# Kernel tuning notes

Measured on AMD Instinct MI355X. Metric: run time of the kernel, lower is better.

The kernel has to match this reference:

```python
import jax, jax.numpy as jnp
from jax import lax
import numpy as np

P_NUM = 63
CHANNEL = 64
KSIZE = 5
PAD = KSIZE // 2
MEAN = jnp.linspace(-310.0, 310.0, P_NUM).reshape(1, 1, P_NUM, 1, 1)
DN = ('NCHW', 'OIHW', 'NCHW')


def rep_pad(x, p=PAD):
    return jnp.pad(x, ((0, 0), (0, 0), (p, p), (p, p)), mode='edge')


def conv(x, w, b):
    out = lax.conv_general_dilated(x, w, (1, 1), 'VALID', dimension_numbers=DN)
    return out + b[None, :, None, None]


def conv_transpose(x, w):
    # torch conv_transpose2d with weight (in, out, k, k), stride 1, no pad ==
    # full correlation with spatially flipped, in/out-transposed kernel
    k = jnp.flip(w, (-2, -1)).transpose(1, 0, 2, 3)  # (out, in, k, k)
    kh = KSIZE - 1
    return lax.conv_general_dilated(x, k, (1, 1), [(kh, kh), (kh, kh)], dimension_numbers=DN)


def crop(x, p=PAD):
    return x[:, :, p:-p, p:-p]


def act(x, w, gradient=False):
    # x: (B,C,H,W); w: (1,C,P,1,1); Gaussian-mixture RBF activation
    d = x[:, :, None, :, :] - MEAN                 # (B,C,P,H,W)
    g = jnp.exp(d * d / -200.0)
    if gradient:
        g = g * (d / -100.0)
    return (g * w).sum(axis=2)                     # (B,C,H,W)


def setup_inputs() -> dict:
    key = jax.random.key(0)
    ks = jax.random.split(key, 8)
    B, H, W = 4, 128, 128
    return {
        'x': jax.random.uniform(ks[0], (B, 1, H, W), jnp.float32),
        'y': jax.random.uniform(ks[1], (B, 1, H, W), jnp.float32),
        'lam': 0,
        'f0': jax.random.normal(ks[2], (CHANNEL, 1, KSIZE, KSIZE), jnp.float32) * 0.1,
        'b0': jax.random.normal(ks[3], (CHANNEL,), jnp.float32) * 0.01,
        'f1': jax.random.normal(ks[4], (1, CHANNEL, KSIZE, KSIZE), jnp.float32) * 0.1,
        'b1': jax.random.normal(ks[5], (1,), jnp.float32) * 0.01,
        'w0': jax.random.normal(ks[6], (1, CHANNEL, P_NUM, 1, 1), jnp.float32) * 0.1,
        'w1': jax.random.normal(ks[7], (1, 1, P_NUM, 1, 1), jnp.float32) * 0.1,
        'lam_param': jnp.float32(np.log(0.1)),
    }


def reference(x, y, lam, f0, b0, f1, b1, w0, w1, lam_param):
    del lam  # third forward arg is ignored by the original module
    x = x * 255.0
    y = y * 255.0
    xx = x
    # encoder
    c0 = conv(rep_pad(x), f0, b0)        # (B,C,H,W)
    a0 = act(c0, w0)
    c1 = conv(rep_pad(a0), f1, b1)       # (B,1,H,W)
    a1 = act(c1, w1)
    # decoder (gradient-like path)
    d = crop(conv_transpose(a1, f1))     # (B,C,H,W)
    d = d * act(c0, w0, gradient=True)
    d = crop(conv_transpose(d, f0))      # (B,1,H,W)
    out = (xx - (d + jnp.exp(lam_param) * (xx - y))) / 255.0
    return out
```

## Files before the change

kernel.cpp:

```cpp
#include <hip/hip_runtime.h>

#define BSZ 4
#define CH 64
#define IH 128
#define IW 128
#define PN 63
#define TLS 32
#define TLH 36
#define XSD 40
#define NT 64
#define CG 8
#define NG 8
#define NPIX (BSZ*IH*IW)

__device__ __forceinline__ float wsel(const float* __restrict__ wrow, int pc, int j) {
    int p  = pc + j;
    int pi = min(max(p, 0), PN - 1);
    return (p == pi) ? wrow[pi] : 0.0f;
}

__device__ __forceinline__ void act_vg(float vv, const float* __restrict__ wrow,
                                       float& av, float& ag) {
    float pcf = floorf(__fmaf_rn(vv, 0.1f, 31.5f));
    pcf = fminf(fmaxf(pcf, 0.0f), 62.0f);
    const int pc = (int)pcf;
    float d0 = vv - __fmaf_rn(pcf, 10.0f, -310.0f);
    d0 = fminf(fmaxf(d0, -150.0f), 150.0f);
    const float G0 = __expf(d0 * d0 * -0.005f);
    const float T  = __expf(d0 * 0.1f);
    const float Ti = __expf(d0 * -0.1f);
    const float C1 = 0.60653066f, C2 = 0.13533528f, C3 = 0.011108997f, C4 = 4.0867714e-4f;
    float accv, accg;
    {
        float t = wsel(wrow, pc, 0) * G0;
        accv = t; accg = t * d0;
    }
    float Tp = T, Tm = Ti;
    {
        float gc = G0 * C1;
        float tp = wsel(wrow, pc,  1) * (gc * Tp);
        float tm = wsel(wrow, pc, -1) * (gc * Tm);
        accv += tp + tm;
        accg = __fmaf_rn(tp, d0 - 10.0f, accg);
        accg = __fmaf_rn(tm, d0 + 10.0f, accg);
    }
    Tp *= T; Tm *= Ti;
    {
        float gc = G0 * C2;
        float tp = wsel(wrow, pc,  2) * (gc * Tp);
        float tm = wsel(wrow, pc, -2) * (gc * Tm);
        accv += tp + tm;
        accg = __fmaf_rn(tp, d0 - 20.0f, accg);
        accg = __fmaf_rn(tm, d0 + 20.0f, accg);
    }
    Tp *= T; Tm *= Ti;
    {
        float gc = G0 * C3;
        float tp = wsel(wrow, pc,  3) * (gc * Tp);
        float tm = wsel(wrow, pc, -3) * (gc * Tm);
        accv += tp + tm;
        accg = __fmaf_rn(tp, d0 - 30.0f, accg);
        accg = __fmaf_rn(tm, d0 + 30.0f, accg);
    }
    Tp *= T; Tm *= Ti;
    {
        float gc = G0 * C4;
        float tp = wsel(wrow, pc,  4) * (gc * Tp);
        float tm = wsel(wrow, pc, -4) * (gc * Tm);
        accv += tp + tm;
        accg = __fmaf_rn(tp, d0 - 40.0f, accg);
        accg = __fmaf_rn(tm, d0 + 40.0f, accg);
    }
    av = accv;
    ag = accg * -0.01f;
}

__device__ __forceinline__ float act_v(float vv, const float* __restrict__ wrow) {
    float pcf = floorf(__fmaf_rn(vv, 0.1f, 31.5f));
    pcf = fminf(fmaxf(pcf, 0.0f), 62.0f);
    const int pc = (int)pcf;
    float d0 = vv - __fmaf_rn(pcf, 10.0f, -310.0f);
    d0 = fminf(fmaxf(d0, -150.0f), 150.0f);
    const float G0 = __expf(d0 * d0 * -0.005f);
    const float T  = __expf(d0 * 0.1f);
    const float Ti = __expf(d0 * -0.1f);
    const float C1 = 0.60653066f, C2 = 0.13533528f, C3 = 0.011108997f, C4 = 4.0867714e-4f;
    float accv = wsel(wrow, pc, 0) * G0;
    float Tp = T, Tm = Ti;
    accv += G0 * C1 * (wsel(wrow, pc, 1) * Tp + wsel(wrow, pc, -1) * Tm);
    Tp *= T; Tm *= Ti;
    accv += G0 * C2 * (wsel(wrow, pc, 2) * Tp + wsel(wrow, pc, -2) * Tm);
    Tp *= T; Tm *= Ti;
    accv += G0 * C3 * (wsel(wrow, pc, 3) * Tp + wsel(wrow, pc, -3) * Tm);
    Tp *= T; Tm *= Ti;
    accv += G0 * C4 * (wsel(wrow, pc, 4) * Tp + wsel(wrow, pc, -4) * Tm);
    return accv;
}

__global__ __launch_bounds__(256) void kAB(const float* __restrict__ x,
                                           const float* __restrict__ f0,
                                           const float* __restrict__ b0,
                                           const float* __restrict__ w0,
                                           const float* __restrict__ f1,
                                           float* __restrict__ c1p,
                                           float* __restrict__ g0out) {
    __shared__ float xs[XSD * XSD];
    __shared__ float a0s[CG][TLH * TLH];
    __shared__ float w0s[CG][PN];

    const int tile = blockIdx.x;
    const int cgi  = blockIdx.y;
    const int cg   = cgi * CG;
    const int b    = tile >> 4;
    const int t    = tile & 15;
    const int h0   = (t >> 2) * TLS;
    const int w0p  = (t & 3) * TLS;
    const int tid  = threadIdx.x;

    for (int i = tid; i < XSD * XSD; i += 256) {
        int iy = i / XSD, ix = i - iy * XSD;
        int gy = min(max(h0 + iy - 4, 0), IH - 1);
        int gx = min(max(w0p + ix - 4, 0), IW - 1);
        xs[i] = x[((size_t)b * IH + gy) * IW + gx] * 255.0f;
    }
    for (int i = tid; i < CG * PN; i += 256)
        w0s[i / PN][i % PN] = w0[(size_t)cg * PN + i];
    __syncthreads();

    for (int p = tid; p < TLH * TLH; p += 256) {
        const int py = p / TLH, px = p - py * TLH;
        const int gy = h0 + py - 2, gx = w0p + px - 2;
        const int gyc = min(max(gy, 0), IH - 1);
        const int gxc = min(max(gx, 0), IW - 1);
        const bool interior = (gy == gyc) && (gx == gxc);
        const int cy = gyc - h0 + 4, cx = gxc - w0p + 4;

        float win[25];
#pragma unroll
        for (int u = 0; u < 5; ++u)
#pragma unroll
            for (int v = 0; v < 5; ++v)
                win[u * 5 + v] = xs[(cy - 2 + u) * XSD + cx - 2 + v];

#pragma unroll
        for (int cc = 0; cc < CG; ++cc) {
            const int c = cg + cc;
            float acc = b0[c];
#pragma unroll
            for (int k = 0; k < 25; ++k)
                acc = __fmaf_rn(win[k], f0[(size_t)c * 25 + k], acc);
            float av, ag;
            act_vg(acc, w0s[cc], av, ag);
            a0s[cc][p] = av;
            if (interior)
                g0out[(((size_t)b * CH + c) * IH + gy) * IW + gx] = ag;
        }
    }
    __syncthreads();

    const int lx = tid & 15, ly = tid >> 4;
    const int r0 = 2 * ly, c0 = 2 * lx;
    float a00 = 0.f, a01 = 0.f, a10 = 0.f, a11 = 0.f;

#pragma unroll 2
    for (int cc = 0; cc < CG; ++cc) {
        float win[6][6];
#pragma unroll
        for (int r = 0; r < 6; ++r) {
            const float2* rp = (const float2*)&a0s[cc][(r0 + r) * TLH + c0];
            float2 p0 = rp[0], p1 = rp[1], p2 = rp[2];
            win[r][0] = p0.x; win[r][1] = p0.y; win[r][2] = p1.x;
            win[r][3] = p1.y; win[r][4] = p2.x; win[r][5] = p2.y;
        }
#pragma unroll
        for (int u = 0; u < 5; ++u)
#pragma unroll
            for (int v = 0; v < 5; ++v) {
                const float kv = f1[(size_t)(cg + cc) * 25 + u * 5 + v];
                a00 = __fmaf_rn(win[u][v],         kv, a00);
                a01 = __fmaf_rn(win[u][v + 1],     kv, a01);
                a10 = __fmaf_rn(win[u + 1][v],     kv, a10);
                a11 = __fmaf_rn(win[u + 1][v + 1], kv, a11);
            }
    }

    const int oy = h0 + r0, ox = w0p + c0;
    const size_t base = (size_t)cgi * NPIX + ((size_t)b * IH + oy) * IW + ox;
    *(float2*)&c1p[base]      = make_float2(a00, a01);
    *(float2*)&c1p[base + IW] = make_float2(a10, a11);
}

__global__ __launch_bounds__(256) void kCD(const float* __restrict__ c1p,
                                           const float* __restrict__ b1,
                                           const float* __restrict__ w1,
                                           const float* __restrict__ f1,
                                           const float* __restrict__ f0,
                                           const float* __restrict__ g0,
                                           float* __restrict__ d3p) {
    __shared__ float a1s[XSD * XSD];
    __shared__ float dbs[CG][TLH * TLH];
    __shared__ float w1s[PN];

    const int tile = blockIdx.x;
    const int cgi  = blockIdx.y;
    const int cg   = cgi * CG;
    const int b    = tile >> 4;
    const int t    = tile & 15;
    const int h0   = (t >> 2) * TLS;
    const int w0p  = (t & 3) * TLS;
    const int tid  = threadIdx.x;

    if (tid < PN) w1s[tid] = w1[tid];
    __syncthreads();

    const float b1v = b1[0];

    for (int p = tid; p < XSD * XSD; p += 256) {
        int iy = p / XSD, ix = p - iy * XSD;
        int gy = h0 + iy - 4, gx = w0p + ix - 4;
        float v = 0.0f;
        if ((unsigned)gy < IH && (unsigned)gx < IW) {
            const size_t pix = ((size_t)b * IH + gy) * IW + gx;
            float s = b1v;
#pragma unroll
            for (int g = 0; g < NG; ++g) s += c1p[(size_t)g * NPIX + pix];
            v = act_v(s, w1s);
        }
        a1s[p] = v;
    }
    __syncthreads();

    for (int p = tid; p < TLH * TLH; p += 256) {
        const int py = p / TLH, px = p - py * TLH;
        const int gy = h0 + py - 2, gx = w0p + px - 2;
        const bool inb = ((unsigned)gy < IH) && ((unsigned)gx < IW);

        float win[25];
#pragma unroll
        for (int u = 0; u < 5; ++u)
#pragma unroll
            for (int v = 0; v < 5; ++v)
                win[u * 5 + v] = a1s[(py + 4 - u) * XSD + (px + 4 - v)];

#pragma unroll
        for (int cc = 0; cc < CG; ++cc) {
            float out = 0.0f;
            if (inb) {
                const int c = cg + cc;
                float d1 = 0.0f;
#pragma unroll
                for (int k = 0; k < 25; ++k)
                    d1 = __fmaf_rn(win[k], f1[(size_t)c * 25 + k], d1);
                out = d1 * g0[(((size_t)b * CH + c) * IH + gy) * IW + gx];
            }
            dbs[cc][p] = out;
        }
    }
    __syncthreads();

    const int lx = tid & 15, ly = tid >> 4;
    const int r0 = 2 * ly, c0 = 2 * lx;
    float a00 = 0.f, a01 = 0.f, a10 = 0.f, a11 = 0.f;

#pragma unroll 2
    for (int cc = 0; cc < CG; ++cc) {
        float win[6][6];
#pragma unroll
        for (int r = 0; r < 6; ++r) {
            const float2* rp = (const float2*)&dbs[cc][(r0 + r) * TLH + c0];
            float2 p0 = rp[0], p1 = rp[1], p2 = rp[2];
            win[r][0] = p0.x; win[r][1] = p0.y; win[r][2] = p1.x;
            win[r][3] = p1.y; win[r][4] = p2.x; win[r][5] = p2.y;
        }
#pragma unroll
        for (int u = 0; u < 5; ++u)
#pragma unroll
            for (int v = 0; v < 5; ++v) {
                const float kv = f0[(size_t)(cg + cc) * 25 + u * 5 + v];
                a00 = __fmaf_rn(win[4 - u][4 - v], kv, a00);
                a01 = __fmaf_rn(win[4 - u][5 - v], kv, a01);
                a10 = __fmaf_rn(win[5 - u][4 - v], kv, a10);
                a11 = __fmaf_rn(win[5 - u][5 - v], kv, a11);
            }
    }

    const int oy = h0 + r0, ox = w0p + c0;
    const size_t base = (size_t)cgi * NPIX + ((size_t)b * IH + oy) * IW + ox;
    *(float2*)&d3p[base]      = make_float2(a00, a01);
    *(float2*)&d3p[base + IW] = make_float2(a10, a11);
}

__global__ __launch_bounds__(256) void kE(const float* __restrict__ d3p,
                                          const float* __restrict__ x,
                                          const float* __restrict__ y,
                                          const float* __restrict__ lam_param,
                                          float* __restrict__ out) {
    const int pid = blockIdx.x * 256 + threadIdx.x;
    float d3 = 0.0f;
#pragma unroll
    for (int g = 0; g < NG; ++g) d3 += d3p[(size_t)g * NPIX + pid];
    const float elam = __expf(lam_param[0]);
    const float xv = x[pid], yv = y[pid];
    out[pid] = xv - d3 * (1.0f / 255.0f) - elam * (xv - yv);
}

extern "C" void kernel_launch(void* const* d_in, const int* in_sizes, int n_in,
                              void* d_out, int out_size, void* d_ws, size_t ws_size,
                              hipStream_t stream) {
    const float* x   = (const float*)d_in[0];
    const float* y   = (const float*)d_in[1];
    const float* f0  = (const float*)d_in[3];
    const float* b0  = (const float*)d_in[4];
    const float* f1  = (const float*)d_in[5];
    const float* b1  = (const float*)d_in[6];
    const float* w0  = (const float*)d_in[7];
    const float* w1  = (const float*)d_in[8];
    const float* lam = (const float*)d_in[9];
    float* out = (float*)d_out;

    const size_t nch = (size_t)BSZ * CH * IH * IW;
    float* g0  = (float*)d_ws;
    float* c1p = g0 + nch;
    float* d3p = c1p + (size_t)NG * NPIX;

    kAB<<<dim3(NT, NG), 256, 0, stream>>>(x, f0, b0, w0, f1, c1p, g0);
    kCD<<<dim3(NT, NG), 256, 0, stream>>>(c1p, b1, w1, f1, f0, g0, d3p);
    kE <<<NPIX / 256, 256, 0, stream>>>(d3p, x, y, lam, out);
}
```

Measured before the change: 141.8 us.

## Split channel groups finer, precompute a1 in separate kernel, pad RBF weight table

Halves the channels per block (CG 8→4, NG 16) so twice as many blocks run, giving more parallelism and less shared memory per block. The layer-1 activation a1 now has its own pointwise kernel, so kCD no longer re-sums the partials and re-evaluates the activation on every halo tile for every channel group. The RBF weight rows are zero-padded in shared memory, which removes the clamp-and-select bounds logic. The ±4 Gaussian terms are dropped, and the channel loops are fully unrolled. In exchange there is an extra launch, more partial buffers to write and sum, and a small accuracy loss from the truncated activation sum.

```diff
diff --git a/kernel.cpp b/kernel.cpp
--- a/kernel.cpp
+++ b/kernel.cpp
@@ -5,95 +5,62 @@
 #define IH 128
 #define IW 128
 #define PN 63
+#define PNP 72
 #define TLS 32
 #define TLH 36
 #define XSD 40
 #define NT 64
-#define CG 8
-#define NG 8
+#define CG 4
+#define NG 16
 #define NPIX (BSZ*IH*IW)
 
-__device__ __forceinline__ float wsel(const float* __restrict__ wrow, int pc, int j) {
-    int p  = pc + j;
-    int pi = min(max(p, 0), PN - 1);
-    return (p == pi) ? wrow[pi] : 0.0f;
-}
-
-__device__ __forceinline__ void act_vg(float vv, const float* __restrict__ wrow,
+__device__ __forceinline__ void act_vg(float vv, const float* __restrict__ wp,
                                        float& av, float& ag) {
     float pcf = floorf(__fmaf_rn(vv, 0.1f, 31.5f));
     pcf = fminf(fmaxf(pcf, 0.0f), 62.0f);
-    const int pc = (int)pcf;
+    const int pc4 = (int)pcf + 4;
     float d0 = vv - __fmaf_rn(pcf, 10.0f, -310.0f);
     d0 = fminf(fmaxf(d0, -150.0f), 150.0f);
     const float G0 = __expf(d0 * d0 * -0.005f);
     const float T  = __expf(d0 * 0.1f);
     const float Ti = __expf(d0 * -0.1f);
-    const float C1 = 0.60653066f, C2 = 0.13533528f, C3 = 0.011108997f, C4 = 4.0867714e-4f;
-    float accv, accg;
-    {
-        float t = wsel(wrow, pc, 0) * G0;
-        accv = t; accg = t * d0;
-    }
+    float t0 = wp[pc4] * G0;
+    float accv = t0, accg = t0 * d0;
     float Tp = T, Tm = Ti;
-    {
-        float gc = G0 * C1;
-        float tp = wsel(wrow, pc,  1) * (gc * Tp);
-        float tm = wsel(wrow, pc, -1) * (gc * Tm);
-        accv += tp + tm;
-        accg = __fmaf_rn(tp, d0 - 10.0f, accg);
-        accg = __fmaf_rn(tm, d0 + 10.0f, accg);
-    }
+    float gc = G0 * 0.60653066f;
+    float tp = wp[pc4 + 1] * (gc * Tp), tm = wp[pc4 - 1] * (gc * Tm);
+    accv += tp + tm;
+    accg = __fmaf_rn(tp, d0 - 10.0f, __fmaf_rn(tm, d0 + 10.0f, accg));
     Tp *= T; Tm *= Ti;
-    {
-        float gc = G0 * C2;
-        float tp = wsel(wrow, pc,  2) * (gc * Tp);
-        float tm = wsel(wrow, pc, -2) * (gc * Tm);
-        accv += tp + tm;
-        accg = __fmaf_rn(tp, d0 - 20.0f, accg);
-        accg = __fmaf_rn(tm, d0 + 20.0f, accg);
-    }
+    gc = G0 * 0.13533528f;
+    tp = wp[pc4 + 2] * (gc * Tp); tm = wp[pc4 - 2] * (gc * Tm);
+    accv += tp + tm;
+    accg = __fmaf_rn(tp, d0 - 20.0f, __fmaf_rn(tm, d0 + 20.0f, accg));
     Tp *= T; Tm *= Ti;
-    {
-        float gc = G0 * C3;
-        float tp = wsel(wrow, pc,  3) * (gc * Tp);
-        float tm = wsel(wrow, pc, -3) * (gc * Tm);
-        accv += tp + tm;
-        accg = __fmaf_rn(tp, d0 - 30.0f, accg);
-        accg = __fmaf_rn(tm, d0 + 30.0f, accg);
-    }
-    Tp *= T; Tm *= Ti;
-    {
-        float gc = G0 * C4;
-        float tp = wsel(wrow, pc,  4) * (gc * Tp);
-        float tm = wsel(wrow, pc, -4) * (gc * Tm);
-        accv += tp + tm;
-        accg = __fmaf_rn(tp, d0 - 40.0f, accg);
-        accg = __fmaf_rn(tm, d0 + 40.0f, accg);
-    }
+    gc = G0 * 0.011108997f;
+    tp = wp[pc4 + 3] * (gc * Tp); tm = wp[pc4 - 3] * (gc * Tm);
+    accv += tp + tm;
+    accg = __fmaf_rn(tp, d0 - 30.0f, __fmaf_rn(tm, d0 + 30.0f, accg));
     av = accv;
     ag = accg * -0.01f;
 }
 
-__device__ __forceinline__ float act_v(float vv, const float* __restrict__ wrow) {
+__device__ __forceinline__ float act_v(float vv, const float* __restrict__ wp) {
     float pcf = floorf(__fmaf_rn(vv, 0.1f, 31.5f));
     pcf = fminf(fmaxf(pcf, 0.0f), 62.0f);
-    const int pc = (int)pcf;
+    const int pc4 = (int)pcf + 4;
     float d0 = vv - __fmaf_rn(pcf, 10.0f, -310.0f);
     d0 = fminf(fmaxf(d0, -150.0f), 150.0f);
     const float G0 = __expf(d0 * d0 * -0.005f);
     const float T  = __expf(d0 * 0.1f);
     const float Ti = __expf(d0 * -0.1f);
-    const float C1 = 0.60653066f, C2 = 0.13533528f, C3 = 0.011108997f, C4 = 4.0867714e-4f;
-    float accv = wsel(wrow, pc, 0) * G0;
+    float accv = wp[pc4] * G0;
     float Tp = T, Tm = Ti;
-    accv += G0 * C1 * (wsel(wrow, pc, 1) * Tp + wsel(wrow, pc, -1) * Tm);
+    accv += G0 * 0.60653066f  * (wp[pc4 + 1] * Tp + wp[pc4 - 1] * Tm);
     Tp *= T; Tm *= Ti;
-    accv += G0 * C2 * (wsel(wrow, pc, 2) * Tp + wsel(wrow, pc, -2) * Tm);
+    accv += G0 * 0.13533528f  * (wp[pc4 + 2] * Tp + wp[pc4 - 2] * Tm);
     Tp *= T; Tm *= Ti;
-    accv += G0 * C3 * (wsel(wrow, pc, 3) * Tp + wsel(wrow, pc, -3) * Tm);
-    Tp *= T; Tm *= Ti;
-    accv += G0 * C4 * (wsel(wrow, pc, 4) * Tp + wsel(wrow, pc, -4) * Tm);
+    accv += G0 * 0.011108997f * (wp[pc4 + 3] * Tp + wp[pc4 - 3] * Tm);
     return accv;
 }
 
@@ -106,7 +73,7 @@
                                            float* __restrict__ g0out) {
     __shared__ float xs[XSD * XSD];
     __shared__ float a0s[CG][TLH * TLH];
-    __shared__ float w0s[CG][PN];
+    __shared__ float w0ps[CG][PNP];
 
     const int tile = blockIdx.x;
     const int cgi  = blockIdx.y;
@@ -123,8 +90,12 @@
         int gx = min(max(w0p + ix - 4, 0), IW - 1);
         xs[i] = x[((size_t)b * IH + gy) * IW + gx] * 255.0f;
     }
-    for (int i = tid; i < CG * PN; i += 256)
-        w0s[i / PN][i % PN] = w0[(size_t)cg * PN + i];
+    for (int i = tid; i < CG * PNP; i += 256) {
+        int cc = i / PNP, k = i - cc * PNP;
+        float v = 0.0f;
+        if (k >= 4 && k < 4 + PN) v = w0[(size_t)(cg + cc) * PN + (k - 4)];
+        w0ps[cc][k] = v;
+    }
     __syncthreads();
 
     for (int p = tid; p < TLH * TLH; p += 256) {
@@ -150,7 +121,7 @@
             for (int k = 0; k < 25; ++k)
                 acc = __fmaf_rn(win[k], f0[(size_t)c * 25 + k], acc);
             float av, ag;
-            act_vg(acc, w0s[cc], av, ag);
+            act_vg(acc, w0ps[cc], av, ag);
             a0s[cc][p] = av;
             if (interior)
                 g0out[(((size_t)b * CH + c) * IH + gy) * IW + gx] = ag;
@@ -162,7 +133,7 @@
     const int r0 = 2 * ly, c0 = 2 * lx;
     float a00 = 0.f, a01 = 0.f, a10 = 0.f, a11 = 0.f;
 
-#pragma unroll 2
+#pragma unroll
     for (int cc = 0; cc < CG; ++cc) {
         float win[6][6];
 #pragma unroll
@@ -190,16 +161,33 @@
     *(float2*)&c1p[base + IW] = make_float2(a10, a11);
 }
 
-__global__ __launch_bounds__(256) void kCD(const float* __restrict__ c1p,
+__global__ __launch_bounds__(256) void kB2(const float* __restrict__ c1p,
                                            const float* __restrict__ b1,
                                            const float* __restrict__ w1,
+                                           float* __restrict__ a1) {
+    __shared__ float w1p[PNP];
+    const int tid = threadIdx.x;
+    if (tid < PNP) {
+        float v = 0.0f;
+        if (tid >= 4 && tid < 4 + PN) v = w1[tid - 4];
+        w1p[tid] = v;
+    }
+    __syncthreads();
+
+    const int pid = blockIdx.x * 256 + tid;
+    float vv = b1[0];
+#pragma unroll
+    for (int g = 0; g < NG; ++g) vv += c1p[(size_t)g * NPIX + pid];
+    a1[pid] = act_v(vv, w1p);
+}
+
+__global__ __launch_bounds__(256) void kCD(const float* __restrict__ a1,
                                            const float* __restrict__ f1,
                                            const float* __restrict__ f0,
                                            const float* __restrict__ g0,
                                            float* __restrict__ d3p) {
     __shared__ float a1s[XSD * XSD];
     __shared__ float dbs[CG][TLH * TLH];
-    __shared__ float w1s[PN];
 
     const int tile = blockIdx.x;
     const int cgi  = blockIdx.y;
@@ -210,22 +198,12 @@
     const int w0p  = (t & 3) * TLS;
     const int tid  = threadIdx.x;
 
-    if (tid < PN) w1s[tid] = w1[tid];
-    __syncthreads();
-
-    const float b1v = b1[0];
-
     for (int p = tid; p < XSD * XSD; p += 256) {
         int iy = p / XSD, ix = p - iy * XSD;
         int gy = h0 + iy - 4, gx = w0p + ix - 4;
         float v = 0.0f;
-        if ((unsigned)gy < IH && (unsigned)gx < IW) {
-            const size_t pix = ((size_t)b * IH + gy) * IW + gx;
-            float s = b1v;
-#pragma unroll
-            for (int g = 0; g < NG; ++g) s += c1p[(size_t)g * NPIX + pix];
-            v = act_v(s, w1s);
-        }
+        if ((unsigned)gy < IH && (unsigned)gx < IW)
+            v = a1[((size_t)b * IH + gy) * IW + gx];
         a1s[p] = v;
     }
     __syncthreads();
@@ -262,7 +240,7 @@
     const int r0 = 2 * ly, c0 = 2 * lx;
     float a00 = 0.f, a01 = 0.f, a10 = 0.f, a11 = 0.f;
 
-#pragma unroll 2
+#pragma unroll
     for (int cc = 0; cc < CG; ++cc) {
         float win[6][6];
 #pragma unroll
@@ -320,10 +298,12 @@
 
     const size_t nch = (size_t)BSZ * CH * IH * IW;
     float* g0  = (float*)d_ws;
-    float* c1p = g0 + nch;
+    float* a1  = g0 + nch;
+    float* c1p = a1 + NPIX;
     float* d3p = c1p + (size_t)NG * NPIX;
 
     kAB<<<dim3(NT, NG), 256, 0, stream>>>(x, f0, b0, w0, f1, c1p, g0);
-    kCD<<<dim3(NT, NG), 256, 0, stream>>>(c1p, b1, w1, f1, f0, g0, d3p);
+    kB2<<<NPIX / 256, 256, 0, stream>>>(c1p, b1, w1, a1);
+    kCD<<<dim3(NT, NG), 256, 0, stream>>>(a1, f1, f0, g0, d3p);
     kE <<<NPIX / 256, 256, 0, stream>>>(d3p, x, y, lam, out);
 }
```

Result: faster. 122.0 us (-13.9%).
